# Optimization experiments

Measured on AMD Instinct MI355X. Metric: run time of the kernel, lower is better.

Reference implementation:

```python
import jax, jax.numpy as jnp
import numpy as np

EPS = 1e-5
N_HEADS = 4
N_GROUPS = 32


def group_norm(x, gamma, beta, num_groups):
    # x: (B, C, H, W)
    B, C, H, W = x.shape
    xg = x.reshape(B, num_groups, (C // num_groups) * H * W)
    mean = xg.mean(axis=2, keepdims=True)
    var = xg.var(axis=2, keepdims=True)
    xn = ((xg - mean) * jax.lax.rsqrt(var + EPS)).reshape(B, C, H, W)
    return xn * gamma[None, :, None, None] + beta[None, :, None, None]


def conv1x1(x, W, b=None):
    # 1x1 conv == channel-mixing matmul: (O,C) x (B,C,H,W) -> (B,O,H,W)
    y = jnp.einsum('oc,bchw->bohw', W, x)
    if b is not None:
        y = y + b[None, :, None, None]
    return y


def setup_inputs() -> dict:
    key = jax.random.key(0)
    ks = jax.random.split(key, 8)
    B, Cq, Cc, H, W = 2, 128, 128, 64, 64
    x = jax.random.normal(ks[0], (B, Cq, H, W), dtype=jnp.float32)
    context = jax.random.normal(ks[1], (B, Cc, H, W), dtype=jnp.float32)
    sq = Cq ** -0.5
    sc = Cc ** -0.5
    return {
        'x': x,
        'context': context,
        'gq': jnp.ones((Cq,), jnp.float32),
        'bq': jnp.zeros((Cq,), jnp.float32),
        'gctx': jnp.ones((Cc,), jnp.float32),
        'bctx': jnp.zeros((Cc,), jnp.float32),
        'Wq': jax.random.normal(ks[2], (Cq, Cq), jnp.float32) * sq,
        'Wk': jax.random.normal(ks[3], (Cq, Cc), jnp.float32) * sc,
        'Wv': jax.random.normal(ks[4], (Cq, Cc), jnp.float32) * sc,
        'Wout': jax.random.normal(ks[5], (Cq, Cq), jnp.float32) * 0.02,
        'bout': jnp.zeros((Cq,), jnp.float32),
        'alpha': jnp.asarray(1.0, jnp.float32),
    }


def reference(x, context, gq, bq, gctx, bctx, Wq, Wk, Wv, Wout, bout, alpha):
    B, C, H, W = x.shape
    hd = C // N_HEADS
    # QKV projections (GroupNorm + 1x1 conv); note v uses raw context (no norm)
    q = conv1x1(group_norm(x, gq, bq, N_GROUPS), Wq)
    k = conv1x1(group_norm(context, gctx, bctx, N_GROUPS), Wk)
    v = conv1x1(context, Wv)
    q = q.reshape(B, N_HEADS, hd, H * W)
    k = k.reshape(B, N_HEADS, hd, H * W)
    v = v.reshape(B, N_HEADS, hd, H * W)
    scale = jnp.asarray(hd ** 0.5, x.dtype)
    attn = jnp.einsum('bncd,bnce->bnde', q, k) / scale  # (B, nH, HW, HW)
    attn = jax.nn.softmax(attn, axis=-1)
    out = jnp.einsum('bnde,bnce->bncd', attn, v).reshape(B, C, H, W)
    return x + alpha * conv1x1(out, Wout, bout)
```

## Files before the change

### kernel.cpp

```cpp
#include <hip/hip_runtime.h>
#include <hip/hip_bf16.h>
#include <math.h>

#define L 4096
#define C 128
#define NH 4
#define HD 32
#define KS 4
#define EPSV 1e-5f

typedef short bf16x8 __attribute__((ext_vector_type(8)));
typedef float f32x4 __attribute__((ext_vector_type(4)));

static __device__ __forceinline__ unsigned pack2bf(float a, float b) {
    __hip_bfloat162 h = __float22bfloat162_rn(make_float2(a, b));
    unsigned u; __builtin_memcpy(&u, &h, 4); return u;
}
static __device__ __forceinline__ float bf_lo(unsigned u) {
    unsigned v = u << 16; float f; __builtin_memcpy(&f, &v, 4); return f;
}
static __device__ __forceinline__ float bf_hi(unsigned u) {
    unsigned v = u & 0xffff0000u; float f; __builtin_memcpy(&f, &v, 4); return f;
}
static __device__ __forceinline__ float fast_exp2(float x) {
    float t = fmaf(x, 8388608.f, 1064992212.f);
    int i = (int)t;
    float r; __builtin_memcpy(&r, &i, 4);
    return r;
}

__global__ __launch_bounds__(256) void gn_stats_kernel(
    const float* __restrict__ x, const float* __restrict__ ctx,
    float* __restrict__ stats)
{
    int bid = blockIdx.x;
    int t = threadIdx.x;
    const float* in = (bid < 64) ? x : ctx;
    int rem = bid & 63;
    const float4* p = (const float4*)(in + (size_t)rem * 16384);
    float s = 0.f, s2 = 0.f;
    #pragma unroll
    for (int rr = 0; rr < 4; rr++) {
        float4 v = p[t + rr * 256];
        s  += v.x + v.y + v.z + v.w;
        s2 += v.x*v.x + v.y*v.y + v.z*v.z + v.w*v.w;
    }
    #pragma unroll
    for (int rr = 0; rr < 4; rr++) {
        float4 v = p[t + 1024 + rr * 256];
        s  += v.x + v.y + v.z + v.w;
        s2 += v.x*v.x + v.y*v.y + v.z*v.z + v.w*v.w;
    }
    #pragma unroll
    for (int rr = 0; rr < 4; rr++) {
        float4 v = p[t + 2048 + rr * 256];
        s  += v.x + v.y + v.z + v.w;
        s2 += v.x*v.x + v.y*v.y + v.z*v.z + v.w*v.w;
    }
    #pragma unroll
    for (int rr = 0; rr < 4; rr++) {
        float4 v = p[t + 3072 + rr * 256];
        s  += v.x + v.y + v.z + v.w;
        s2 += v.x*v.x + v.y*v.y + v.z*v.z + v.w*v.w;
    }
    #pragma unroll
    for (int m = 32; m >= 1; m >>= 1) {
        s  += __shfl_xor(s, m);
        s2 += __shfl_xor(s2, m);
    }
    __shared__ float wsum[4][2];
    int w = t >> 6;
    if ((t & 63) == 0) { wsum[w][0] = s; wsum[w][1] = s2; }
    __syncthreads();
    if (t == 0) {
        float S = wsum[0][0] + wsum[1][0] + wsum[2][0] + wsum[3][0];
        float S2 = wsum[0][1] + wsum[1][1] + wsum[2][1] + wsum[3][1];
        float mean = S * (1.f / 16384.f);
        float var = S2 * (1.f / 16384.f) - mean * mean;
        stats[bid * 2]     = mean;
        stats[bid * 2 + 1] = rsqrtf(var + EPSV);
    }
}

__global__ __launch_bounds__(256) void proj_kernel(
    const float* __restrict__ x, const float* __restrict__ ctx,
    const float* __restrict__ gq, const float* __restrict__ bq,
    const float* __restrict__ gctx, const float* __restrict__ bctx,
    const float* __restrict__ stats,
    const float* __restrict__ Wq, const float* __restrict__ Wk,
    const float* __restrict__ Wv,
    unsigned short* __restrict__ Qt, unsigned short* __restrict__ Kt,
    unsigned short* __restrict__ Vsw)
{
    int t = threadIdx.x;
    int w = t >> 6, lane = t & 63, n16 = lane & 15, quad = lane >> 4;
    int dtile = blockIdx.x * 32;
    int b = blockIdx.y, z = blockIdx.z;

    const float* in; const float* Wm; const float* gamma; const float* beta;
    int sel = 1, donorm = 1; float oscale = 1.f;
    if (z == 0)      { in = x;   Wm = Wq; gamma = gq;   beta = bq;   sel = 0;
                       oscale = 0.17677669529663689f * 1.4426950408889634f; }
    else if (z == 1) { in = ctx; Wm = Wk; gamma = gctx; beta = bctx; }
    else             { in = ctx; Wm = Wv; gamma = 0;    beta = 0;    donorm = 0; }

    __shared__ __attribute__((aligned(16))) unsigned short Xs[32 * 136];

    {
        int c0 = (t >> 3) * 4, d4 = (t & 7) * 4;
        const float* inb = in + (size_t)b * (C * L);
        float vv[4][4];
        #pragma unroll
        for (int j = 0; j < 4; j++) {
            int c = c0 + j;
            float sc = 1.f, sh = 0.f;
            if (donorm) {
                int sidx = (sel * 64 + b * 32 + (c >> 2)) * 2;
                float mean = stats[sidx], inv = stats[sidx + 1];
                sc = inv * gamma[c];
                sh = beta[c] - mean * sc;
            }
            float4 v = *(const float4*)(inb + (size_t)c * L + dtile + d4);
            vv[j][0] = v.x * sc + sh; vv[j][1] = v.y * sc + sh;
            vv[j][2] = v.z * sc + sh; vv[j][3] = v.w * sc + sh;
        }
        #pragma unroll
        for (int i = 0; i < 4; i++) {
            uint2 pk;
            pk.x = pack2bf(vv[0][i], vv[1][i]);
            pk.y = pack2bf(vv[2][i], vv[3][i]);
            *(uint2*)&Xs[(d4 + i) * 136 + c0] = pk;
        }
    }

    bf16x8 wa[2][4];
    #pragma unroll
    for (int os2 = 0; os2 < 2; os2++) {
        const float* wr = Wm + (size_t)(((w + os2 * 4) * 16) + n16) * C + quad * 8;
        #pragma unroll
        for (int kk = 0; kk < 4; kk++) {
            float4 a  = *(const float4*)(wr + kk * 32);
            float4 b2 = *(const float4*)(wr + kk * 32 + 4);
            unsigned u4[4] = { pack2bf(a.x, a.y),  pack2bf(a.z, a.w),
                               pack2bf(b2.x, b2.y), pack2bf(b2.z, b2.w) };
            __builtin_memcpy(&wa[os2][kk], u4, 16);
        }
    }
    __syncthreads();

    f32x4 zero = {0.f, 0.f, 0.f, 0.f};
    f32x4 acc[2][2];
    acc[0][0] = zero; acc[0][1] = zero; acc[1][0] = zero; acc[1][1] = zero;
    #pragma unroll
    for (int kk = 0; kk < 4; kk++) {
        #pragma unroll
        for (int dg = 0; dg < 2; dg++) {
            bf16x8 xb;
            uint4 u = *(const uint4*)&Xs[(dg * 16 + n16) * 136 + kk * 32 + quad * 8];
            __builtin_memcpy(&xb, &u, 16);
            acc[0][dg] = __builtin_amdgcn_mfma_f32_16x16x32_bf16(wa[0][kk], xb, acc[0][dg], 0, 0, 0);
            acc[1][dg] = __builtin_amdgcn_mfma_f32_16x16x32_bf16(wa[1][kk], xb, acc[1][dg], 0, 0, 0);
        }
    }

    #pragma unroll
    for (int os2 = 0; os2 < 2; os2++) {
        int o = ((w + os2 * 4) * 16) + quad * 4;
        int h = o >> 5, c32 = o & 31;
        #pragma unroll
        for (int dg = 0; dg < 2; dg++) {
            int d = dtile + dg * 16 + n16;
            if (z < 2) {
                unsigned short* outp = (z == 0) ? Qt : Kt;
                uint2 pk;
                pk.x = pack2bf(acc[os2][dg][0] * oscale, acc[os2][dg][1] * oscale);
                pk.y = pack2bf(acc[os2][dg][2] * oscale, acc[os2][dg][3] * oscale);
                *(uint2*)(outp + ((size_t)(b * NH + h) * L + d) * HD + c32) = pk;
            } else {
                unsigned short* vb = Vsw + (size_t)(b * NH + h) * (L * HD)
                                   + (size_t)(d >> 3) * 256 + (d & 7);
                #pragma unroll
                for (int r = 0; r < 4; r++) {
                    __hip_bfloat16 hv = __float2bfloat16(acc[os2][dg][r]);
                    unsigned short us; __builtin_memcpy(&us, &hv, 2);
                    vb[(c32 + r) * 8] = us;
                }
            }
        }
    }
}

__global__ __launch_bounds__(256, 4) void flash_kernel(
    const unsigned short* __restrict__ Qt, const unsigned short* __restrict__ Kt,
    const unsigned short* __restrict__ Vsw, unsigned short* __restrict__ Po,
    float* __restrict__ Pl)
{
    __shared__ __attribute__((aligned(16))) unsigned short Ps[4 * 2 * 16 * 72];

    int t = threadIdx.x;
    int w = t >> 6, lane = t & 63;
    int n16 = lane & 15, quad = lane >> 4;
    int bh = blockIdx.x;
    int qbase = blockIdx.y * 128 + w * 32;
    int ks = blockIdx.z;
    size_t hb = (size_t)bh * (L * HD);

    bf16x8 qf[2];
    #pragma unroll
    for (int sp = 0; sp < 2; sp++) {
        uint4 u = *(const uint4*)(Qt + hb + (size_t)(qbase + sp * 16 + n16) * HD + quad * 8);
        __builtin_memcpy(&qf[sp], &u, 16);
    }

    bf16x8 onesf;
    #pragma unroll
    for (int j = 0; j < 8; j++) onesf[j] = (short)0x3F80;

    const unsigned short* kfp = Kt + hb + (size_t)n16 * HD + quad * 8;
    const unsigned short* vfp = Vsw + hb + quad * 256 + n16 * 8;

    int e0 = ks * (L / KS);

    bf16x8 ka[2][4];
    #pragma unroll
    for (int et = 0; et < 4; et++) {
        uint4 u = *(const uint4*)(kfp + (size_t)(e0 + et * 16) * HD);
        __builtin_memcpy(&ka[0][et], &u, 16);
    }

    f32x4 zero = {0.f, 0.f, 0.f, 0.f};
    f32x4 oacc[2][2], lacc[2];
    oacc[0][0] = zero; oacc[0][1] = zero; oacc[1][0] = zero; oacc[1][1] = zero;
    lacc[0] = zero; lacc[1] = zero;

    #pragma unroll 2
    for (int kt = 0; kt < L / KS / 64; kt++) {
        int cur = kt & 1, nxt = cur ^ 1;
        int ecur = e0 + kt * 64;
        #pragma unroll
        for (int et = 0; et < 4; et++) {
            uint4 u = *(const uint4*)(kfp + (size_t)(ecur + 64 + et * 16) * HD);
            __builtin_memcpy(&ka[nxt][et], &u, 16);
        }
        bf16x8 va[4];
        #pragma unroll
        for (int es = 0; es < 2; es++)
            #pragma unroll
            for (int f = 0; f < 2; f++) {
                uint4 u = *(const uint4*)(vfp + (size_t)(ecur + es * 32) * 32 + f * 128);
                __builtin_memcpy(&va[es * 2 + f], &u, 16);
            }

        #pragma unroll
        for (int sp = 0; sp < 2; sp++) {
            f32x4 s[4];
            #pragma unroll
            for (int et = 0; et < 4; et++)
                s[et] = __builtin_amdgcn_mfma_f32_16x16x32_bf16(ka[cur][et], qf[sp], zero, 0, 0, 0);
            unsigned short* pw = Ps + ((w * 2 + sp) * 1152) + n16 * 72;
            #pragma unroll
            for (int et = 0; et < 4; et++) {
                uint2 pk;
                pk.x = pack2bf(fast_exp2(s[et][0]), fast_exp2(s[et][1]));
                pk.y = pack2bf(fast_exp2(s[et][2]), fast_exp2(s[et][3]));
                *(uint2*)(pw + et * 16 + quad * 4) = pk;
            }
        }

        #pragma unroll
        for (int sp = 0; sp < 2; sp++) {
            unsigned short* pw = Ps + ((w * 2 + sp) * 1152) + n16 * 72;
            #pragma unroll
            for (int es = 0; es < 2; es++) {
                bf16x8 pf;
                uint4 u = *(const uint4*)(pw + es * 32 + quad * 8);
                __builtin_memcpy(&pf, &u, 16);
                oacc[sp][0] = __builtin_amdgcn_mfma_f32_16x16x32_bf16(va[es * 2 + 0], pf, oacc[sp][0], 0, 0, 0);
                oacc[sp][1] = __builtin_amdgcn_mfma_f32_16x16x32_bf16(va[es * 2 + 1], pf, oacc[sp][1], 0, 0, 0);
                lacc[sp]    = __builtin_amdgcn_mfma_f32_16x16x32_bf16(onesf, pf, lacc[sp], 0, 0, 0);
            }
        }
    }

    #pragma unroll
    for (int sp = 0; sp < 2; sp++) {
        int dq = qbase + sp * 16 + n16;
        unsigned short* po = Po + ((size_t)(bh * KS + ks) * L + dq) * 32;
        uint2 pk0, pk1;
        pk0.x = pack2bf(oacc[sp][0][0], oacc[sp][0][1]);
        pk0.y = pack2bf(oacc[sp][0][2], oacc[sp][0][3]);
        pk1.x = pack2bf(oacc[sp][1][0], oacc[sp][1][1]);
        pk1.y = pack2bf(oacc[sp][1][2], oacc[sp][1][3]);
        *(uint2*)(po + quad * 4)      = pk0;
        *(uint2*)(po + 16 + quad * 4) = pk1;
        if (quad == 0)
            Pl[(size_t)(bh * KS + ks) * L + dq] = lacc[sp][0];
    }
}

__global__ __launch_bounds__(256) void final_kernel(
    const unsigned short* __restrict__ Po, const float* __restrict__ Pl,
    const float* __restrict__ x, const float* __restrict__ Wout,
    const float* __restrict__ bout, const float* __restrict__ alpha,
    float* __restrict__ out)
{
    int t = threadIdx.x;
    int w = t >> 6, lane = t & 63, n16 = lane & 15, quad = lane >> 4;
    int dtile = blockIdx.x * 16;
    int b = blockIdx.y;

    __shared__ __attribute__((aligned(16))) float Ot[128 * 20];
    unsigned short* Xs = (unsigned short*)Ot;

    {
        int d_l = t >> 4, c0 = (t & 15) * 8;
        int dq = dtile + d_l;
        int bh = b * NH + (c0 >> 5);
        int c32 = c0 & 31;
        float l = 0.f;
        float o8[8] = {0.f, 0.f, 0.f, 0.f, 0.f, 0.f, 0.f, 0.f};
        #pragma unroll
        for (int ks = 0; ks < KS; ks++) {
            size_t base = (size_t)(bh * KS + ks) * L + dq;
            l += Pl[base];
            uint4 u = *(const uint4*)(Po + base * 32 + c32);
            o8[0] += bf_lo(u.x); o8[1] += bf_hi(u.x);
            o8[2] += bf_lo(u.y); o8[3] += bf_hi(u.y);
            o8[4] += bf_lo(u.z); o8[5] += bf_hi(u.z);
            o8[6] += bf_lo(u.w); o8[7] += bf_hi(u.w);
        }
        float rl = 1.f / l;
        uint4 pk;
        pk.x = pack2bf(o8[0] * rl, o8[1] * rl);
        pk.y = pack2bf(o8[2] * rl, o8[3] * rl);
        pk.z = pack2bf(o8[4] * rl, o8[5] * rl);
        pk.w = pack2bf(o8[6] * rl, o8[7] * rl);
        *(uint4*)&Xs[d_l * 136 + c0] = pk;
    }

    bf16x8 wa[2][4];
    #pragma unroll
    for (int os2 = 0; os2 < 2; os2++) {
        const float* wr = Wout + (size_t)(((w + os2 * 4) * 16) + n16) * C + quad * 8;
        #pragma unroll
        for (int kk = 0; kk < 4; kk++) {
            float4 a  = *(const float4*)(wr + kk * 32);
            float4 b2 = *(const float4*)(wr + kk * 32 + 4);
            unsigned u4[4] = { pack2bf(a.x, a.y),  pack2bf(a.z, a.w),
                               pack2bf(b2.x, b2.y), pack2bf(b2.z, b2.w) };
            __builtin_memcpy(&wa[os2][kk], u4, 16);
        }
    }
    __syncthreads();

    f32x4 zero = {0.f, 0.f, 0.f, 0.f};
    f32x4 acc[2];
    acc[0] = zero; acc[1] = zero;
    #pragma unroll
    for (int kk = 0; kk < 4; kk++) {
        bf16x8 xb;
        uint4 u = *(const uint4*)&Xs[n16 * 136 + kk * 32 + quad * 8];
        __builtin_memcpy(&xb, &u, 16);
        acc[0] = __builtin_amdgcn_mfma_f32_16x16x32_bf16(wa[0][kk], xb, acc[0], 0, 0, 0);
        acc[1] = __builtin_amdgcn_mfma_f32_16x16x32_bf16(wa[1][kk], xb, acc[1], 0, 0, 0);
    }
    __syncthreads();

    #pragma unroll
    for (int os2 = 0; os2 < 2; os2++) {
        int o = ((w + os2 * 4) * 16) + quad * 4;
        #pragma unroll
        for (int r = 0; r < 4; r++)
            Ot[(o + r) * 20 + n16] = acc[os2][r];
    }
    __syncthreads();

    float al = alpha[0];
    int o = t >> 1, dh = (t & 1) * 8;
    float bo = bout[o];
    const float* xb2 = x + ((size_t)b * C + o) * L + dtile + dh;
    float* ob = out + ((size_t)b * C + o) * L + dtile + dh;
    #pragma unroll
    for (int jj = 0; jj < 2; jj++) {
        float4 a  = *(const float4*)&Ot[o * 20 + dh + jj * 4];
        float4 xv = *(const float4*)(xb2 + jj * 4);
        float4 r;
        r.x = xv.x + al * (a.x + bo);
        r.y = xv.y + al * (a.y + bo);
        r.z = xv.z + al * (a.z + bo);
        r.w = xv.w + al * (a.w + bo);
        *(float4*)(ob + jj * 4) = r;
    }
}

extern "C" void kernel_launch(void* const* d_in, const int* in_sizes, int n_in,
                              void* d_out, int out_size, void* d_ws, size_t ws_size,
                              hipStream_t stream) {
    const float* x     = (const float*)d_in[0];
    const float* ctx   = (const float*)d_in[1];
    const float* gq    = (const float*)d_in[2];
    const float* bq    = (const float*)d_in[3];
    const float* gctx  = (const float*)d_in[4];
    const float* bctx  = (const float*)d_in[5];
    const float* Wq    = (const float*)d_in[6];
    const float* Wk    = (const float*)d_in[7];
    const float* Wv    = (const float*)d_in[8];
    const float* Wout  = (const float*)d_in[9];
    const float* bout  = (const float*)d_in[10];
    const float* alpha = (const float*)d_in[11];
    float* out = (float*)d_out;

    char* ws = (char*)d_ws;
    unsigned short* Qt  = (unsigned short*)(ws);
    unsigned short* Kt  = (unsigned short*)(ws + 2097152);
    unsigned short* Vsw = (unsigned short*)(ws + 4194304);
    unsigned short* Po  = (unsigned short*)(ws + 6291456);
    float*          Pl  = (float*)(ws + 14680064);
    float*          stats = (float*)(ws + 15204352);

    gn_stats_kernel<<<128, 256, 0, stream>>>(x, ctx, stats);
    proj_kernel<<<dim3(128, 2, 3), 256, 0, stream>>>(x, ctx, gq, bq, gctx, bctx,
                                                     stats, Wq, Wk, Wv, Qt, Kt, Vsw);
    flash_kernel<<<dim3(8, 32, KS), 256, 0, stream>>>(Qt, Kt, Vsw, Po, Pl);
    final_kernel<<<dim3(256, 2), 256, 0, stream>>>(Po, Pl, x, Wout, bout, alpha, out);
}
```

Measured before the change: 128.1 us.

## Stage K tiles through shared memory and double-buffer V loads in flash kernel

Before, each of the four waves loaded the whole K tile from global memory into its own registers. Now the block loads each 64-key K tile once, cooperatively, into a double-buffered shared-memory array that all waves read from. V fragments are also prefetched one iteration ahead into a register double buffer, so their global loads overlap with compute. The cost is an extra shared-memory buffer, a __syncthreads per iteration, and more registers for the prefetched V. The last iteration prefetches K and V one tile past the key split, which may read out of range at the final split.

Result: no change. 128.4 us (+0.2%).

```diff
diff --git a/kernel.cpp b/kernel.cpp
--- a/kernel.cpp
+++ b/kernel.cpp
@@ -195,7 +195,8 @@
     const unsigned short* __restrict__ Vsw, unsigned short* __restrict__ Po,
     float* __restrict__ Pl)
 {
-    __shared__ __attribute__((aligned(16))) unsigned short Ps[4 * 2 * 16 * 72];
+    __shared__ __attribute__((aligned(16))) unsigned short Ksh[2][2048];
+    __shared__ __attribute__((aligned(16))) unsigned short Ps[4 * 2 * 1152];
 
     int t = threadIdx.x;
     int w = t >> 6, lane = t & 63;
@@ -216,47 +217,55 @@
     #pragma unroll
     for (int j = 0; j < 8; j++) onesf[j] = (short)0x3F80;
 
-    const unsigned short* kfp = Kt + hb + (size_t)n16 * HD + quad * 8;
+    int e0 = ks * (L / KS);
+    const unsigned short* kgp = Kt + hb + (size_t)e0 * HD + t * 8;
     const unsigned short* vfp = Vsw + hb + quad * 256 + n16 * 8;
-
-    int e0 = ks * (L / KS);
-
-    bf16x8 ka[2][4];
-    #pragma unroll
-    for (int et = 0; et < 4; et++) {
-        uint4 u = *(const uint4*)(kfp + (size_t)(e0 + et * 16) * HD);
-        __builtin_memcpy(&ka[0][et], &u, 16);
-    }
 
     f32x4 zero = {0.f, 0.f, 0.f, 0.f};
     f32x4 oacc[2][2], lacc[2];
     oacc[0][0] = zero; oacc[0][1] = zero; oacc[1][0] = zero; oacc[1][1] = zero;
     lacc[0] = zero; lacc[1] = zero;
 
+    {
+        uint4 k0 = *(const uint4*)kgp;
+        *(uint4*)&Ksh[0][t * 8] = k0;
+    }
+    bf16x8 va[2][4];
+    #pragma unroll
+    for (int es = 0; es < 2; es++)
+        #pragma unroll
+        for (int f = 0; f < 2; f++) {
+            uint4 u = *(const uint4*)(vfp + (size_t)(e0 + es * 32) * 32 + f * 128);
+            __builtin_memcpy(&va[0][es * 2 + f], &u, 16);
+        }
+    __syncthreads();
+
     #pragma unroll 2
     for (int kt = 0; kt < L / KS / 64; kt++) {
         int cur = kt & 1, nxt = cur ^ 1;
-        int ecur = e0 + kt * 64;
-        #pragma unroll
-        for (int et = 0; et < 4; et++) {
-            uint4 u = *(const uint4*)(kfp + (size_t)(ecur + 64 + et * 16) * HD);
-            __builtin_memcpy(&ka[nxt][et], &u, 16);
-        }
-        bf16x8 va[4];
+        int enxt = e0 + (kt + 1) * 64;
+        uint4 kr2 = *(const uint4*)(kgp + (kt + 1) * 2048);
         #pragma unroll
         for (int es = 0; es < 2; es++)
             #pragma unroll
             for (int f = 0; f < 2; f++) {
-                uint4 u = *(const uint4*)(vfp + (size_t)(ecur + es * 32) * 32 + f * 128);
-                __builtin_memcpy(&va[es * 2 + f], &u, 16);
+                uint4 u = *(const uint4*)(vfp + (size_t)(enxt + es * 32) * 32 + f * 128);
+                __builtin_memcpy(&va[nxt][es * 2 + f], &u, 16);
             }
+
+        bf16x8 ka[4];
+        #pragma unroll
+        for (int et = 0; et < 4; et++) {
+            uint4 u = *(const uint4*)&Ksh[cur][(et * 16 + n16) * 32 + quad * 8];
+            __builtin_memcpy(&ka[et], &u, 16);
+        }
 
         #pragma unroll
         for (int sp = 0; sp < 2; sp++) {
             f32x4 s[4];
             #pragma unroll
             for (int et = 0; et < 4; et++)
-                s[et] = __builtin_amdgcn_mfma_f32_16x16x32_bf16(ka[cur][et], qf[sp], zero, 0, 0, 0);
+                s[et] = __builtin_amdgcn_mfma_f32_16x16x32_bf16(ka[et], qf[sp], zero, 0, 0, 0);
             unsigned short* pw = Ps + ((w * 2 + sp) * 1152) + n16 * 72;
             #pragma unroll
             for (int et = 0; et < 4; et++) {
@@ -275,11 +284,14 @@
                 bf16x8 pf;
                 uint4 u = *(const uint4*)(pw + es * 32 + quad * 8);
                 __builtin_memcpy(&pf, &u, 16);
-                oacc[sp][0] = __builtin_amdgcn_mfma_f32_16x16x32_bf16(va[es * 2 + 0], pf, oacc[sp][0], 0, 0, 0);
-                oacc[sp][1] = __builtin_amdgcn_mfma_f32_16x16x32_bf16(va[es * 2 + 1], pf, oacc[sp][1], 0, 0, 0);
+                oacc[sp][0] = __builtin_amdgcn_mfma_f32_16x16x32_bf16(va[cur][es * 2 + 0], pf, oacc[sp][0], 0, 0, 0);
+                oacc[sp][1] = __builtin_amdgcn_mfma_f32_16x16x32_bf16(va[cur][es * 2 + 1], pf, oacc[sp][1], 0, 0, 0);
                 lacc[sp]    = __builtin_amdgcn_mfma_f32_16x16x32_bf16(onesf, pf, lacc[sp], 0, 0, 0);
             }
         }
+
+        *(uint4*)&Ksh[nxt][t * 8] = kr2;
+        __syncthreads();
     }
 
     #pragma unroll
```

## Split GroupNorm stats over more blocks and double-buffer V loads in flash kernel

Applied to the files above, without the earlier changes.

The GroupNorm statistics kernel now launches 512 blocks, each summing a quarter of a group, and writes raw sums. The projection kernel combines the four partials into mean and inverse std itself. The flash kernel also prefetches V fragments for the next key tile into a double buffer, as it already did for K. This adds parallelism to the small stats pass and hides V load latency, at the cost of more registers in the flash kernel and possible occupancy pressure.

Measured after the change: 127.8 us. About the same (-0.3%).

```diff
diff --git a/kernel.cpp b/kernel.cpp
--- a/kernel.cpp
+++ b/kernel.cpp
@@ -35,31 +35,14 @@
 {
     int bid = blockIdx.x;
     int t = threadIdx.x;
-    const float* in = (bid < 64) ? x : ctx;
-    int rem = bid & 63;
-    const float4* p = (const float4*)(in + (size_t)rem * 16384);
+    const float* in = (bid < 256) ? x : ctx;
+    int idx = bid & 255;
+    const float4* p = (const float4*)(in + (size_t)(idx >> 2) * 16384
+                                         + (size_t)(idx & 3) * 4096);
     float s = 0.f, s2 = 0.f;
     #pragma unroll
     for (int rr = 0; rr < 4; rr++) {
         float4 v = p[t + rr * 256];
-        s  += v.x + v.y + v.z + v.w;
-        s2 += v.x*v.x + v.y*v.y + v.z*v.z + v.w*v.w;
-    }
-    #pragma unroll
-    for (int rr = 0; rr < 4; rr++) {
-        float4 v = p[t + 1024 + rr * 256];
-        s  += v.x + v.y + v.z + v.w;
-        s2 += v.x*v.x + v.y*v.y + v.z*v.z + v.w*v.w;
-    }
-    #pragma unroll
-    for (int rr = 0; rr < 4; rr++) {
-        float4 v = p[t + 2048 + rr * 256];
-        s  += v.x + v.y + v.z + v.w;
-        s2 += v.x*v.x + v.y*v.y + v.z*v.z + v.w*v.w;
-    }
-    #pragma unroll
-    for (int rr = 0; rr < 4; rr++) {
-        float4 v = p[t + 3072 + rr * 256];
         s  += v.x + v.y + v.z + v.w;
         s2 += v.x*v.x + v.y*v.y + v.z*v.z + v.w*v.w;
     }
@@ -73,12 +56,10 @@
     if ((t & 63) == 0) { wsum[w][0] = s; wsum[w][1] = s2; }
     __syncthreads();
     if (t == 0) {
-        float S = wsum[0][0] + wsum[1][0] + wsum[2][0] + wsum[3][0];
+        float S  = wsum[0][0] + wsum[1][0] + wsum[2][0] + wsum[3][0];
         float S2 = wsum[0][1] + wsum[1][1] + wsum[2][1] + wsum[3][1];
-        float mean = S * (1.f / 16384.f);
-        float var = S2 * (1.f / 16384.f) - mean * mean;
-        stats[bid * 2]     = mean;
-        stats[bid * 2 + 1] = rsqrtf(var + EPSV);
+        stats[bid * 2]     = S;
+        stats[bid * 2 + 1] = S2;
     }
 }
 
@@ -109,20 +90,31 @@
     {
         int c0 = (t >> 3) * 4, d4 = (t & 7) * 4;
         const float* inb = in + (size_t)b * (C * L);
+        float sc0 = 1.f, sh0 = 0.f;
+        float scg[4], shg[4];
+        if (donorm) {
+            int gl = (sel * 256 + (b * 32 + (c0 >> 2)) * 4) * 2;
+            float S  = stats[gl] + stats[gl + 2] + stats[gl + 4] + stats[gl + 6];
+            float S2 = stats[gl + 1] + stats[gl + 3] + stats[gl + 5] + stats[gl + 7];
+            float mean = S * (1.f / 16384.f);
+            float var  = S2 * (1.f / 16384.f) - mean * mean;
+            float inv  = rsqrtf(var + EPSV);
+            #pragma unroll
+            for (int j = 0; j < 4; j++) {
+                scg[j] = inv * gamma[c0 + j];
+                shg[j] = beta[c0 + j] - mean * scg[j];
+            }
+        } else {
+            #pragma unroll
+            for (int j = 0; j < 4; j++) { scg[j] = 1.f; shg[j] = 0.f; }
+        }
+        (void)sc0; (void)sh0;
         float vv[4][4];
         #pragma unroll
         for (int j = 0; j < 4; j++) {
-            int c = c0 + j;
-            float sc = 1.f, sh = 0.f;
-            if (donorm) {
-                int sidx = (sel * 64 + b * 32 + (c >> 2)) * 2;
-                float mean = stats[sidx], inv = stats[sidx + 1];
-                sc = inv * gamma[c];
-                sh = beta[c] - mean * sc;
-            }
-            float4 v = *(const float4*)(inb + (size_t)c * L + dtile + d4);
-            vv[j][0] = v.x * sc + sh; vv[j][1] = v.y * sc + sh;
-            vv[j][2] = v.z * sc + sh; vv[j][3] = v.w * sc + sh;
+            float4 v = *(const float4*)(inb + (size_t)(c0 + j) * L + dtile + d4);
+            vv[j][0] = v.x * scg[j] + shg[j]; vv[j][1] = v.y * scg[j] + shg[j];
+            vv[j][2] = v.z * scg[j] + shg[j]; vv[j][3] = v.w * scg[j] + shg[j];
         }
         #pragma unroll
         for (int i = 0; i < 4; i++) {
@@ -195,7 +187,7 @@
     const unsigned short* __restrict__ Vsw, unsigned short* __restrict__ Po,
     float* __restrict__ Pl)
 {
-    __shared__ __attribute__((aligned(16))) unsigned short Ps[4 * 2 * 16 * 72];
+    __shared__ __attribute__((aligned(16))) unsigned short Ps[4 * 2 * 1152];
 
     int t = threadIdx.x;
     int w = t >> 6, lane = t & 63;
@@ -221,12 +213,19 @@
 
     int e0 = ks * (L / KS);
 
-    bf16x8 ka[2][4];
+    bf16x8 ka[2][4], va[2][4];
     #pragma unroll
     for (int et = 0; et < 4; et++) {
         uint4 u = *(const uint4*)(kfp + (size_t)(e0 + et * 16) * HD);
         __builtin_memcpy(&ka[0][et], &u, 16);
     }
+    #pragma unroll
+    for (int es = 0; es < 2; es++)
+        #pragma unroll
+        for (int f = 0; f < 2; f++) {
+            uint4 u = *(const uint4*)(vfp + (size_t)(e0 + es * 32) * 32 + f * 128);
+            __builtin_memcpy(&va[0][es * 2 + f], &u, 16);
+        }
 
     f32x4 zero = {0.f, 0.f, 0.f, 0.f};
     f32x4 oacc[2][2], lacc[2];
@@ -236,19 +235,18 @@
     #pragma unroll 2
     for (int kt = 0; kt < L / KS / 64; kt++) {
         int cur = kt & 1, nxt = cur ^ 1;
-        int ecur = e0 + kt * 64;
+        int enxt = e0 + (kt + 1) * 64;
         #pragma unroll
         for (int et = 0; et < 4; et++) {
-            uint4 u = *(const uint4*)(kfp + (size_t)(ecur + 64 + et * 16) * HD);
+            uint4 u = *(const uint4*)(kfp + (size_t)(enxt + et * 16) * HD);
             __builtin_memcpy(&ka[nxt][et], &u, 16);
         }
-        bf16x8 va[4];
         #pragma unroll
         for (int es = 0; es < 2; es++)
             #pragma unroll
             for (int f = 0; f < 2; f++) {
-                uint4 u = *(const uint4*)(vfp + (size_t)(ecur + es * 32) * 32 + f * 128);
-                __builtin_memcpy(&va[es * 2 + f], &u, 16);
+                uint4 u = *(const uint4*)(vfp + (size_t)(enxt + es * 32) * 32 + f * 128);
+                __builtin_memcpy(&va[nxt][es * 2 + f], &u, 16);
             }
 
         #pragma unroll
@@ -275,8 +273,8 @@
                 bf16x8 pf;
                 uint4 u = *(const uint4*)(pw + es * 32 + quad * 8);
                 __builtin_memcpy(&pf, &u, 16);
-                oacc[sp][0] = __builtin_amdgcn_mfma_f32_16x16x32_bf16(va[es * 2 + 0], pf, oacc[sp][0], 0, 0, 0);
-                oacc[sp][1] = __builtin_amdgcn_mfma_f32_16x16x32_bf16(va[es * 2 + 1], pf, oacc[sp][1], 0, 0, 0);
+                oacc[sp][0] = __builtin_amdgcn_mfma_f32_16x16x32_bf16(va[cur][es * 2 + 0], pf, oacc[sp][0], 0, 0, 0);
+                oacc[sp][1] = __builtin_amdgcn_mfma_f32_16x16x32_bf16(va[cur][es * 2 + 1], pf, oacc[sp][1], 0, 0, 0);
                 lacc[sp]    = __builtin_amdgcn_mfma_f32_16x16x32_bf16(onesf, pf, lacc[sp], 0, 0, 0);
             }
         }
@@ -418,7 +416,7 @@
     float*          Pl  = (float*)(ws + 14680064);
     float*          stats = (float*)(ws + 15204352);
 
-    gn_stats_kernel<<<128, 256, 0, stream>>>(x, ctx, stats);
+    gn_stats_kernel<<<512, 256, 0, stream>>>(x, ctx, stats);
     proj_kernel<<<dim3(128, 2, 3), 256, 0, stream>>>(x, ctx, gq, bq, gctx, bctx,
                                                      stats, Wq, Wk, Wv, Qt, Kt, Vsw);
     flash_kernel<<<dim3(8, 32, KS), 256, 0, stream>>>(Qt, Kt, Vsw, Po, Pl);
```
